# Performance work log

Hardware: AMD Instinct MI355X
Metric: run time of the kernel (lower is better)

Reference implementation:

```python
import jax, jax.numpy as jnp
import numpy as np

KSIZE = 13
BETA = 0.97
THR = 1.0
SMIN, SMAX = 0.4, 10.0


def gaussian_kernel(sigma):
    # matches torch: coarse grid [-6,6] (13 pts), normalized by sum over fine grid [-60,60] (130 pts)
    r = jnp.linspace(-(KSIZE // 2), KSIZE // 2, KSIZE)
    r_all = jnp.linspace(-(KSIZE // 2) * 10.0, (KSIZE // 2) * 10.0, KSIZE * 10)
    k = jnp.exp(-0.5 * (r / sigma) ** 2)
    norm = jnp.sum(jnp.exp(-0.5 * (r_all / sigma) ** 2))
    return k / norm


def setup_inputs() -> dict:
    key = jax.random.key(0)
    k1, = jax.random.split(key, 1)
    B, C, T = 512, 224, 224
    inp = jax.random.normal(k1, (B, 1, C, T), dtype=jnp.float32)
    w = jnp.float32((SMIN + SMAX) / 2.0)  # 5.2, init value of nn.Parameter
    return {"inp": inp, "w": w}


def reference(inp, w):
    x = inp[:, 0]                      # (B, C, T)
    B, C, T = x.shape
    wc = jnp.clip(w, SMIN, SMAX)
    kern = gaussian_kernel(wc)          # (K,), symmetric
    pad = (KSIZE - 1) // 2

    # gaussian smoothing across the channel axis, same kernel for every t and b
    # x_mean[b,c,t] = sum_k kern[k] * pad_C(x)[b, c+k, t]
    xc = x.transpose(0, 2, 1).reshape(B * T, 1, C)   # (B*T, 1, C)
    xm = jax.lax.conv_general_dilated(
        xc, kern.reshape(1, 1, KSIZE),
        window_strides=(1,), padding=[(pad, pad)],
        dimension_numbers=("NCH", "OIH", "NCH"))
    x_mean = xm.reshape(B, T, C).transpose(0, 2, 1)  # (B, C, T)

    # input current: clip x at the smoothed mean from above
    I = x - jax.nn.relu(x - x_mean)                   # (B, C, T)

    # snn.Leaky (beta=0.97, threshold=1, reset_mechanism='subtract')
    def step(mem, I_t):
        reset = (mem > THR).astype(mem.dtype)         # reset based on previous mem
        mem = BETA * mem + I_t - reset * THR
        spk = (mem > THR).astype(mem.dtype)           # Heaviside(mem - threshold)
        return mem, spk

    mem0 = jnp.zeros((B, C), x.dtype)
    _, spk = jax.lax.scan(step, mem0, I.transpose(2, 0, 1))  # (T, B, C)
    spk = spk.transpose(1, 2, 0)[:, None]                    # (B, 1, C, T)
    return spk
```

## Files before the change

### kernel.cpp

```cpp
#include <hip/hip_runtime.h>

constexpr int Cc   = 224;
constexpr int Tt   = 224;
constexpr int TT   = 32;
constexpr int NT   = Tt / TT;
constexpr int ROWS = 236;
constexpr int BUFW = ROWS * TT;
constexpr int BDIM = 256;

#define GLDS16(src, dst) __builtin_amdgcn_global_load_lds( \
    (const __attribute__((address_space(1))) unsigned int*)(src), \
    (__attribute__((address_space(3))) unsigned int*)(dst), 16, 0, 0)


__global__ __launch_bounds__(BDIM, 2)
void cgss_snn_kernel(const float* __restrict__ x,
                     const float* __restrict__ wp,
                     float* __restrict__ out)
{
    __shared__ float lds[2 * BUFW];

    const int tid = threadIdx.x;
    const int w   = tid >> 6;
    const int l   = tid & 63;
    const int b   = blockIdx.x;
    const long long bofs = (long long)b * (Cc * Tt);
    const float* xb = x + bofs;
    float*       ob = out + bofs;

    if (tid < 192) {
        int bufi = tid / 96;
        int q    = tid - 96 * bufi;
        int rr   = q >> 3;
        int slot = q & 7;
        int row  = (rr < 6) ? rr : (224 + rr);
        float4 z = make_float4(0.f, 0.f, 0.f, 0.f);
        *reinterpret_cast<float4*>(&lds[bufi * BUFW + row * 32 + slot * 4]) = z;
    }

    const int srow = l >> 3;
    const int stq  = (l & 7) ^ ((6 + srow) & 7);
    auto stage = [&](int bufi, int t0) {
        float* base = &lds[bufi * BUFW];
#pragma unroll
        for (int i = 0; i < 7; ++i) {
            int j   = 7 * w + i;
            int row = 6 + 8 * j + srow;
            const float* src = xb + (row - 6) * Tt + t0 + stq * 4;
            GLDS16(src, &base[(6 + 8 * j) * 32]);
        }
    };

    stage(0, 0);

    float kr[13];
    {
        float wv = wp[0];
        float wc = fminf(fmaxf(wv, 0.4f), 10.0f);
        float norm = 0.0f;
        const float step = 120.0f / 129.0f;
        for (int j = 0; j < 130; ++j) {
            float r = -60.0f + (float)j * step;
            float z = r / wc;
            norm += expf(-0.5f * z * z);
        }
        for (int i = 0; i < 13; ++i) {
            float r = (float)(i - 6);
            float z = r / wc;
            kr[i] = expf(-0.5f * z * z) / norm;
        }
    }

    float mem = 0.0f, rstv = 0.0f;
    int bufc = 0;

    asm volatile("s_waitcnt vmcnt(0)" ::: "memory");
    __syncthreads();

    for (int tile = 0; tile < NT; ++tile) {
        const int t0 = tile * TT;
        if (tile < NT - 1) stage(bufc ^ 1, t0 + TT);

        unsigned m = 0;
        if (tid < Cc) {
            const char* sb = (const char*)&lds[bufc * BUFW];
#pragma unroll 2
            for (int tq = 0; tq < 8; ++tq) {
                float4 v[13];
#pragma unroll
                for (int k = 0; k < 13; ++k) {
                    int row = tid + k;
                    v[k] = *reinterpret_cast<const float4*>(
                        sb + row * 128 + ((tq ^ (row & 7)) << 4));
                }
                float4 acc = make_float4(0.f, 0.f, 0.f, 0.f);
#pragma unroll
                for (int k = 0; k < 13; ++k) {
                    float kk = kr[k];
                    acc.x += kk * v[k].x;  acc.y += kk * v[k].y;
                    acc.z += kk * v[k].z;  acc.w += kk * v[k].w;
                }
                const float* xv = (const float*)&v[6];
                const float* av = (const float*)&acc;
#pragma unroll
                for (int s = 0; s < 4; ++s) {
                    float d  = xv[s] - av[s];
                    float rl = d > 0.0f ? d : 0.0f;
                    float I  = xv[s] - rl;
                    mem = 0.97f * mem + I - rstv;
                    bool sp = mem > 1.0f;
                    rstv = sp ? 1.0f : 0.0f;
                    m |= sp ? (1u << (4 * tq + s)) : 0u;
                }
            }
        }
        __syncthreads();

        if (tid < Cc) {
            char* sb = (char*)&lds[bufc * BUFW];
#pragma unroll
            for (int tq = 0; tq < 8; ++tq) {
                float4 sv;
                sv.x = (m >> (4 * tq + 0)) & 1 ? 1.0f : 0.0f;
                sv.y = (m >> (4 * tq + 1)) & 1 ? 1.0f : 0.0f;
                sv.z = (m >> (4 * tq + 2)) & 1 ? 1.0f : 0.0f;
                sv.w = (m >> (4 * tq + 3)) & 1 ? 1.0f : 0.0f;
                *reinterpret_cast<float4*>(
                    sb + tid * 128 + ((tq ^ (tid & 7)) << 4)) = sv;
            }
        }
        __syncthreads();

        {
            const char* sb = (const char*)&lds[bufc * BUFW];
            const int s = l & 7;
#pragma unroll
            for (int i = 0; i < 7; ++i) {
                int cr = 8 * (7 * w + i) + (l >> 3);
                float4 v = *reinterpret_cast<const float4*>(
                    sb + cr * 128 + ((s ^ (cr & 7)) << 4));
                *reinterpret_cast<float4*>(&ob[(long long)cr * Tt + t0 + 4 * s]) = v;
            }
        }

        asm volatile("s_waitcnt vmcnt(0)" ::: "memory");
        __syncthreads();
        bufc ^= 1;
    }
}

extern "C" void kernel_launch(void* const* d_in, const int* in_sizes, int n_in,
                              void* d_out, int out_size, void* d_ws, size_t ws_size,
                              hipStream_t stream)
{
    const float* x  = (const float*)d_in[0];
    const float* w  = (const float*)d_in[1];
    float* out      = (float*)d_out;
    const int B = in_sizes[0] / (Cc * Tt);
    cgss_snn_kernel<<<B, BDIM, 0, stream>>>(x, w, out);
}
```

Measured before the change: 75.36 us.

## Split channel convolution into register-reuse sliding window phase before the LIF scan

```diff
diff --git a/kernel.cpp b/kernel.cpp
--- a/kernel.cpp
+++ b/kernel.cpp
@@ -7,6 +7,7 @@
 constexpr int ROWS = 236;
 constexpr int BUFW = ROWS * TT;
 constexpr int BDIM = 256;
+constexpr int CPG  = 28;
 
 #define GLDS16(src, dst) __builtin_amdgcn_global_load_lds( \
     (const __attribute__((address_space(1))) unsigned int*)(src), \
@@ -39,14 +40,13 @@
     }
 
     const int srow = l >> 3;
-    const int stq  = (l & 7) ^ ((6 + srow) & 7);
+    const int scol = l & 7;
     auto stage = [&](int bufi, int t0) {
         float* base = &lds[bufi * BUFW];
 #pragma unroll
         for (int i = 0; i < 7; ++i) {
-            int j   = 7 * w + i;
-            int row = 6 + 8 * j + srow;
-            const float* src = xb + (row - 6) * Tt + t0 + stq * 4;
+            int j = 7 * w + i;
+            const float* src = xb + (8 * j + srow) * Tt + t0 + scol * 4;
             GLDS16(src, &base[(6 + 8 * j) * 32]);
         }
     };
@@ -71,6 +71,12 @@
         }
     }
 
+    const int g     = tid >> 5;
+    const int l5    = tid & 31;
+    const int rowA0 = CPG * g;
+    const int rowB  = tid + 6;
+    const int pB    = rowB & 7;
+
     float mem = 0.0f, rstv = 0.0f;
     int bufc = 0;
 
@@ -81,52 +87,59 @@
         const int t0 = tile * TT;
         if (tile < NT - 1) stage(bufc ^ 1, t0 + TT);
 
-        unsigned m = 0;
-        if (tid < Cc) {
-            const char* sb = (const char*)&lds[bufc * BUFW];
-#pragma unroll 2
-            for (int tq = 0; tq < 8; ++tq) {
-                float4 v[13];
+        float acc[CPG], ctr[CPG];
+        {
+            const float* sb = &lds[bufc * BUFW] + rowA0 * 32 + l5;
 #pragma unroll
-                for (int k = 0; k < 13; ++k) {
-                    int row = tid + k;
-                    v[k] = *reinterpret_cast<const float4*>(
-                        sb + row * 128 + ((tq ^ (row & 7)) << 4));
+            for (int j = 0; j < CPG; ++j) acc[j] = 0.0f;
+#pragma unroll
+            for (int r = 0; r < CPG + 12; ++r) {
+                float xv = sb[r * 32];
+#pragma unroll
+                for (int j = 0; j < CPG; ++j) {
+                    int i = r - j;
+                    if (i == 6) ctr[j] = xv;
+                    if (i >= 0 && i < 13) acc[j] += kr[i] * xv;
                 }
-                float4 acc = make_float4(0.f, 0.f, 0.f, 0.f);
+            }
 #pragma unroll
-                for (int k = 0; k < 13; ++k) {
-                    float kk = kr[k];
-                    acc.x += kk * v[k].x;  acc.y += kk * v[k].y;
-                    acc.z += kk * v[k].z;  acc.w += kk * v[k].w;
-                }
-                const float* xv = (const float*)&v[6];
-                const float* av = (const float*)&acc;
+            for (int j = 0; j < CPG; ++j) {
+                float xv = ctr[j];
+                float d  = xv - acc[j];
+                float rl = d > 0.0f ? d : 0.0f;
+                acc[j]   = xv - rl;
+            }
+        }
+        __syncthreads();
+
+        {
+            float* sb = &lds[bufc * BUFW];
+            const int q = l5 >> 2, lo = l5 & 3;
 #pragma unroll
-                for (int s = 0; s < 4; ++s) {
-                    float d  = xv[s] - av[s];
-                    float rl = d > 0.0f ? d : 0.0f;
-                    float I  = xv[s] - rl;
-                    mem = 0.97f * mem + I - rstv;
-                    bool sp = mem > 1.0f;
-                    rstv = sp ? 1.0f : 0.0f;
-                    m |= sp ? (1u << (4 * tq + s)) : 0u;
-                }
+            for (int j = 0; j < CPG; ++j) {
+                int row = rowA0 + 6 + j;
+                sb[row * 32 + ((q ^ (row & 7)) << 2) + lo] = acc[j];
             }
         }
         __syncthreads();
 
         if (tid < Cc) {
-            char* sb = (char*)&lds[bufc * BUFW];
+            char* sb = (char*)&lds[bufc * BUFW] + rowB * 128;
 #pragma unroll
             for (int tq = 0; tq < 8; ++tq) {
-                float4 sv;
-                sv.x = (m >> (4 * tq + 0)) & 1 ? 1.0f : 0.0f;
-                sv.y = (m >> (4 * tq + 1)) & 1 ? 1.0f : 0.0f;
-                sv.z = (m >> (4 * tq + 2)) & 1 ? 1.0f : 0.0f;
-                sv.w = (m >> (4 * tq + 3)) & 1 ? 1.0f : 0.0f;
-                *reinterpret_cast<float4*>(
-                    sb + tid * 128 + ((tq ^ (tid & 7)) << 4)) = sv;
+                char* p = sb + ((tq ^ pB) << 4);
+                float4 v = *reinterpret_cast<const float4*>(p);
+                float4 s4;
+                float* vv = (float*)&v;
+                float* ss = (float*)&s4;
+#pragma unroll
+                for (int s = 0; s < 4; ++s) {
+                    mem = 0.97f * mem + vv[s] - rstv;
+                    bool sp = mem > 1.0f;
+                    rstv = sp ? 1.0f : 0.0f;
+                    ss[s] = sp ? 1.0f : 0.0f;
+                }
+                *reinterpret_cast<float4*>(p) = s4;
             }
         }
         __syncthreads();
@@ -136,14 +149,15 @@
             const int s = l & 7;
 #pragma unroll
             for (int i = 0; i < 7; ++i) {
-                int cr = 8 * (7 * w + i) + (l >> 3);
+                int row = 6 + 8 * (7 * w + i) + (l >> 3);
                 float4 v = *reinterpret_cast<const float4*>(
-                    sb + cr * 128 + ((s ^ (cr & 7)) << 4));
-                *reinterpret_cast<float4*>(&ob[(long long)cr * Tt + t0 + 4 * s]) = v;
+                    sb + row * 128 + ((s ^ (row & 7)) << 4));
+                *reinterpret_cast<float4*>(
+                    &ob[(long long)(row - 6) * Tt + t0 + 4 * s]) = v;
             }
         }
 
-        asm volatile("s_waitcnt vmcnt(0)" ::: "memory");
+        asm volatile("s_waitcnt vmcnt(7)" ::: "memory");
         __syncthreads();
         bufc ^= 1;
     }
```

After: 135.6 us. 80.0% more time.

## Replace LDS-direct loads with register-staged prefetch and padded LDS rows

Applied to the files above, without the earlier changes.

```diff
diff --git a/kernel.cpp b/kernel.cpp
--- a/kernel.cpp
+++ b/kernel.cpp
@@ -4,14 +4,10 @@
 constexpr int Tt   = 224;
 constexpr int TT   = 32;
 constexpr int NT   = Tt / TT;
+constexpr int LDW  = 36;
 constexpr int ROWS = 236;
-constexpr int BUFW = ROWS * TT;
+constexpr int BUFW = ROWS * LDW;
 constexpr int BDIM = 256;
-
-#define GLDS16(src, dst) __builtin_amdgcn_global_load_lds( \
-    (const __attribute__((address_space(1))) unsigned int*)(src), \
-    (__attribute__((address_space(3))) unsigned int*)(dst), 16, 0, 0)
-
 
 __global__ __launch_bounds__(BDIM, 2)
 void cgss_snn_kernel(const float* __restrict__ x,
@@ -23,8 +19,7 @@
     const int tid = threadIdx.x;
     const int w   = tid >> 6;
     const int l   = tid & 63;
-    const int b   = blockIdx.x;
-    const long long bofs = (long long)b * (Cc * Tt);
+    const long long bofs = (long long)blockIdx.x * (Cc * Tt);
     const float* xb = x + bofs;
     float*       ob = out + bofs;
 
@@ -34,24 +29,19 @@
         int rr   = q >> 3;
         int slot = q & 7;
         int row  = (rr < 6) ? rr : (224 + rr);
-        float4 z = make_float4(0.f, 0.f, 0.f, 0.f);
-        *reinterpret_cast<float4*>(&lds[bufi * BUFW + row * 32 + slot * 4]) = z;
+        *reinterpret_cast<float4*>(&lds[bufi * BUFW + row * LDW + slot * 4]) =
+            make_float4(0.f, 0.f, 0.f, 0.f);
     }
 
     const int srow = l >> 3;
-    const int stq  = (l & 7) ^ ((6 + srow) & 7);
-    auto stage = [&](int bufi, int t0) {
-        float* base = &lds[bufi * BUFW];
+    const int stq  = l & 7;
+    const int rowbase = 56 * w + srow;
+
+    float4 vst[7];
 #pragma unroll
-        for (int i = 0; i < 7; ++i) {
-            int j   = 7 * w + i;
-            int row = 6 + 8 * j + srow;
-            const float* src = xb + (row - 6) * Tt + t0 + stq * 4;
-            GLDS16(src, &base[(6 + 8 * j) * 32]);
-        }
-    };
-
-    stage(0, 0);
+    for (int i = 0; i < 7; ++i)
+        vst[i] = *reinterpret_cast<const float4*>(
+            xb + (rowbase + 8 * i) * Tt + 4 * stq);
 
     float kr[13];
     {
@@ -71,28 +61,37 @@
         }
     }
 
-    float mem = 0.0f, rstv = 0.0f;
+#pragma unroll
+    for (int i = 0; i < 7; ++i)
+        *reinterpret_cast<float4*>(
+            &lds[(rowbase + 8 * i + 6) * LDW + 4 * stq]) = vst[i];
+#pragma unroll
+    for (int i = 0; i < 7; ++i)
+        vst[i] = *reinterpret_cast<const float4*>(
+            xb + (rowbase + 8 * i) * Tt + TT + 4 * stq);
+
+    asm volatile("s_waitcnt lgkmcnt(0)" ::: "memory");
+    __builtin_amdgcn_s_barrier();
+    __builtin_amdgcn_sched_barrier(0);
+
+    float mem = 0.f, rstv = 0.f;
     int bufc = 0;
 
-    asm volatile("s_waitcnt vmcnt(0)" ::: "memory");
-    __syncthreads();
-
+#pragma unroll 1
     for (int tile = 0; tile < NT; ++tile) {
         const int t0 = tile * TT;
-        if (tile < NT - 1) stage(bufc ^ 1, t0 + TT);
+        float* cur = &lds[bufc * BUFW];
+        float* nxt = &lds[(bufc ^ 1) * BUFW];
 
         unsigned m = 0;
         if (tid < Cc) {
-            const char* sb = (const char*)&lds[bufc * BUFW];
-#pragma unroll 2
+            const float* base = cur + tid * LDW;
+#pragma unroll
             for (int tq = 0; tq < 8; ++tq) {
                 float4 v[13];
 #pragma unroll
-                for (int k = 0; k < 13; ++k) {
-                    int row = tid + k;
-                    v[k] = *reinterpret_cast<const float4*>(
-                        sb + row * 128 + ((tq ^ (row & 7)) << 4));
-                }
+                for (int k = 0; k < 13; ++k)
+                    v[k] = *reinterpret_cast<const float4*>(base + k * LDW + 4 * tq);
                 float4 acc = make_float4(0.f, 0.f, 0.f, 0.f);
 #pragma unroll
                 for (int k = 0; k < 13; ++k) {
@@ -114,37 +113,48 @@
                 }
             }
         }
-        __syncthreads();
+
+        asm volatile("s_waitcnt lgkmcnt(0)" ::: "memory");
+        __builtin_amdgcn_s_barrier();
+        __builtin_amdgcn_sched_barrier(0);
 
         if (tid < Cc) {
-            char* sb = (char*)&lds[bufc * BUFW];
+            float* sp = cur + (tid + 6) * LDW;
 #pragma unroll
             for (int tq = 0; tq < 8; ++tq) {
-                float4 sv;
-                sv.x = (m >> (4 * tq + 0)) & 1 ? 1.0f : 0.0f;
-                sv.y = (m >> (4 * tq + 1)) & 1 ? 1.0f : 0.0f;
-                sv.z = (m >> (4 * tq + 2)) & 1 ? 1.0f : 0.0f;
-                sv.w = (m >> (4 * tq + 3)) & 1 ? 1.0f : 0.0f;
-                *reinterpret_cast<float4*>(
-                    sb + tid * 128 + ((tq ^ (tid & 7)) << 4)) = sv;
+                float4 s4;
+                s4.x = (m >> (4 * tq + 0)) & 1 ? 1.0f : 0.0f;
+                s4.y = (m >> (4 * tq + 1)) & 1 ? 1.0f : 0.0f;
+                s4.z = (m >> (4 * tq + 2)) & 1 ? 1.0f : 0.0f;
+                s4.w = (m >> (4 * tq + 3)) & 1 ? 1.0f : 0.0f;
+                *reinterpret_cast<float4*>(sp + 4 * tq) = s4;
             }
         }
-        __syncthreads();
-
-        {
-            const char* sb = (const char*)&lds[bufc * BUFW];
-            const int s = l & 7;
+        if (tile < NT - 1) {
 #pragma unroll
-            for (int i = 0; i < 7; ++i) {
-                int cr = 8 * (7 * w + i) + (l >> 3);
-                float4 v = *reinterpret_cast<const float4*>(
-                    sb + cr * 128 + ((s ^ (cr & 7)) << 4));
-                *reinterpret_cast<float4*>(&ob[(long long)cr * Tt + t0 + 4 * s]) = v;
-            }
+            for (int i = 0; i < 7; ++i)
+                *reinterpret_cast<float4*>(
+                    &nxt[(rowbase + 8 * i + 6) * LDW + 4 * stq]) = vst[i];
+        }
+        if (tile < NT - 2) {
+#pragma unroll
+            for (int i = 0; i < 7; ++i)
+                vst[i] = *reinterpret_cast<const float4*>(
+                    xb + (rowbase + 8 * i) * Tt + t0 + 2 * TT + 4 * stq);
         }
 
-        asm volatile("s_waitcnt vmcnt(0)" ::: "memory");
-        __syncthreads();
+        asm volatile("s_waitcnt lgkmcnt(0)" ::: "memory");
+        __builtin_amdgcn_s_barrier();
+        __builtin_amdgcn_sched_barrier(0);
+
+#pragma unroll
+        for (int i = 0; i < 7; ++i) {
+            int cr = rowbase + 8 * i;
+            float4 v = *reinterpret_cast<const float4*>(
+                &cur[(cr + 6) * LDW + 4 * stq]);
+            *reinterpret_cast<float4*>(&ob[(long long)cr * Tt + t0 + 4 * stq]) = v;
+        }
+
         bufc ^= 1;
     }
 }
```

After: 89.18 us. 18.3% more time.
